# Performance work log

Hardware: AMD Instinct MI355X
Metric: run time of the kernel (lower is better)

The kernel has to match this reference:

```python
import jax, jax.numpy as jnp
import numpy as np

# Layer widths of the hardcoded torch MLP: 2->128->256->512->512->512->512->256->128->3
_DIMS = [2, 128, 256, 512, 512, 512, 512, 256, 128, 3]


def setup_inputs() -> dict:
    key = jax.random.key(0)
    keys = jax.random.split(key, 2 * (len(_DIMS) - 1) + 1)
    inp = {"x": jax.random.uniform(keys[0], (1048576, 2), dtype=jnp.float32)}
    for i in range(len(_DIMS) - 1):
        fan_in, fan_out = _DIMS[i], _DIMS[i + 1]
        bound = 1.0 / np.sqrt(fan_in)  # torch nn.Linear default init range
        inp[f"W{i+1}"] = jax.random.uniform(keys[2 * i + 1], (fan_in, fan_out), jnp.float32, -bound, bound)
        inp[f"b{i+1}"] = jax.random.uniform(keys[2 * i + 2], (fan_out,), jnp.float32, -bound, bound)
    return inp


def reference(x, W1, b1, W2, b2, W3, b3, W4, b4, W5, b5, W6, b6, W7, b7, W8, b8, W9, b9):
    # (transpose of torch's [out, in]); math is identical: y = x @ W + b.
    h = x
    for W, b in ((W1, b1), (W2, b2), (W3, b3), (W4, b4),
                 (W5, b5), (W6, b6), (W7, b7), (W8, b8)):
        h = jax.nn.relu(h @ W + b)
    return jax.nn.sigmoid(h @ W9 + b9)
```

## Files before the change

kernel.cpp:

```cpp
#include <hip/hip_runtime.h>

typedef _Float16 f16;
typedef __attribute__((ext_vector_type(4))) _Float16 f16x4;
typedef __attribute__((ext_vector_type(8))) _Float16 f16x8;
typedef __attribute__((ext_vector_type(16))) float f32x16;

#define MT 128
#define NBF 4
#define LDSP 1024

#define OFF2 0
#define OFF3 32768
#define OFF4 163840
#define OFF5 425984
#define OFF6 688128
#define OFF7 950272
#define OFF8 1081344
#define OFF9 1114112
#define TOTAL_FRAG_LANES 139776

__device__ __forceinline__ uint32_t swz(int row, int colbytes) {
  return (uint32_t)(row * LDSP + (colbytes ^ ((row & 31) << 4)));
}

__global__ void repack_kernel(const float* __restrict__ W2, const float* __restrict__ W3,
                              const float* __restrict__ W4, const float* __restrict__ W5,
                              const float* __restrict__ W6, const float* __restrict__ W7,
                              const float* __restrict__ W8, const float* __restrict__ W9,
                              f16* __restrict__ ws) {
  int gid = blockIdx.x * 256 + threadIdx.x;
  if (gid >= TOTAL_FRAG_LANES) return;
  const float* src; int N, NT; size_t dst; int local;
  if      (gid <   4096) { src = W2; N = 256; NT = 8;  dst = OFF2; local = gid;          }
  else if (gid <  20480) { src = W3; N = 512; NT = 16; dst = OFF3; local = gid -   4096; }
  else if (gid <  53248) { src = W4; N = 512; NT = 16; dst = OFF4; local = gid -  20480; }
  else if (gid <  86016) { src = W5; N = 512; NT = 16; dst = OFF5; local = gid -  53248; }
  else if (gid < 118784) { src = W6; N = 512; NT = 16; dst = OFF6; local = gid -  86016; }
  else if (gid < 135168) { src = W7; N = 256; NT = 8;  dst = OFF7; local = gid - 118784; }
  else if (gid < 139264) { src = W8; N = 128; NT = 4;  dst = OFF8; local = gid - 135168; }
  else                   { src = W9; N = 3;   NT = 1;  dst = OFF9; local = gid - 139264; }
  int lane = local & 63;
  int frag = local >> 6;
  int kf = frag / NT, nf = frag % NT;
  int n  = nf * 32 + (lane & 31);
  int kb = kf * 16 + ((lane >> 5) << 3);
  f16x8 v;
  #pragma unroll
  for (int i = 0; i < 8; ++i) {
    float val = (n < N) ? src[(size_t)(kb + i) * N + n] : 0.0f;
    v[i] = (f16)val;
  }
  *reinterpret_cast<f16x8*>(ws + dst + (size_t)local * 8) = v;
}

template<int KT, int MF, int WMG, int WBG>
__device__ __forceinline__ void run_layer(char* act, const f16* __restrict__ wp,
                                          const float* __restrict__ bias) {
  constexpr int FM  = MF / WMG;
  constexpr int FB  = NBF / WBG;
  const int tid   = threadIdx.x;
  const int lane  = tid & 63;
  const int wid   = tid >> 6;
  const int wm    = wid / WBG;
  const int wb    = wid % WBG;
  const int mlane = lane & 31;
  const int h     = lane >> 5;

  f32x16 acc[FM][FB];
  #pragma unroll
  for (int fm = 0; fm < FM; ++fm) {
    const int mbase = (wm * FM + fm) * 32;
    #pragma unroll
    for (int g = 0; g < 4; ++g) {
      const float4 bb = *reinterpret_cast<const float4*>(&bias[mbase + g * 8 + 4 * h]);
      #pragma unroll
      for (int j = 0; j < 4; ++j)
        #pragma unroll
        for (int fb = 0; fb < FB; ++fb)
          acc[fm][fb][g * 4 + j] = ((const float*)&bb)[j];
    }
  }

  const f16x8* __restrict__ wfrag = reinterpret_cast<const f16x8*>(wp);

  #pragma unroll 2
  for (int kf = 0; kf < KT; ++kf) {
    f16x8 a[FM];
    #pragma unroll
    for (int fm = 0; fm < FM; ++fm)
      a[fm] = wfrag[(size_t)(kf * MF + wm * FM + fm) * 64 + lane];
    f16x8 b[FB];
    #pragma unroll
    for (int fb = 0; fb < FB; ++fb)
      b[fb] = *reinterpret_cast<const f16x8*>(
                  act + swz((wb * FB + fb) * 32 + mlane, kf * 32 + h * 16));
    __builtin_amdgcn_s_setprio(1);
    #pragma unroll
    for (int fm = 0; fm < FM; ++fm)
      #pragma unroll
      for (int fb = 0; fb < FB; ++fb)
        acc[fm][fb] = __builtin_amdgcn_mfma_f32_32x32x16_f16(a[fm], b[fb], acc[fm][fb], 0, 0, 0);
    __builtin_amdgcn_s_setprio(0);
  }

  __syncthreads();
  #pragma unroll
  for (int fm = 0; fm < FM; ++fm) {
    const int mbase = (wm * FM + fm) * 32;
    #pragma unroll
    for (int fb = 0; fb < FB; ++fb) {
      const int row = (wb * FB + fb) * 32 + mlane;
      #pragma unroll
      for (int g = 0; g < 4; ++g) {
        const int m0 = mbase + g * 8 + 4 * h;
        f16x4 v;
        #pragma unroll
        for (int j = 0; j < 4; ++j)
          v[j] = (f16)fmaxf(acc[fm][fb][g * 4 + j], 0.0f);
        *reinterpret_cast<f16x4*>(act + swz(row, m0 * 2)) = v;
      }
    }
  }
  __syncthreads();
}

__global__ __launch_bounds__(512, 2)
void mlp_kernel(const float* __restrict__ x,
                const float* __restrict__ W1, const float* __restrict__ b1,
                const f16*   __restrict__ wpk,
                const float* __restrict__ b2, const float* __restrict__ b3,
                const float* __restrict__ b4, const float* __restrict__ b5,
                const float* __restrict__ b6, const float* __restrict__ b7,
                const float* __restrict__ b8, const float* __restrict__ b9,
                float* __restrict__ out) {
  __shared__ __align__(16) char act[MT * LDSP];
  const int row0 = blockIdx.x * MT;
  const int tid  = threadIdx.x;

  {
    const int r  = tid >> 2;
    const int cb = (tid & 3) * 32;
    const float2 xv = reinterpret_cast<const float2*>(x)[row0 + r];
    #pragma unroll
    for (int q = 0; q < 4; ++q) {
      f16x8 v;
      #pragma unroll
      for (int j = 0; j < 8; ++j) {
        int c = cb + q * 8 + j;
        v[j] = (f16)fmaxf(fmaf(xv.y, W1[128 + c], fmaf(xv.x, W1[c], b1[c])), 0.0f);
      }
      *reinterpret_cast<f16x8*>(act + swz(r, cb * 2 + q * 16)) = v;
    }
  }
  __syncthreads();

  run_layer<8,  8,  4, 2>(act, wpk + OFF2, b2);
  run_layer<16, 16, 4, 2>(act, wpk + OFF3, b3);
  for (int rep = 0; rep < 3; ++rep) {
    const float* bias = (rep == 0) ? b4 : (rep == 1) ? b5 : b6;
    run_layer<32, 16, 4, 2>(act, wpk + OFF4 + rep * (OFF5 - OFF4), bias);
  }
  run_layer<32, 8,  4, 2>(act, wpk + OFF7, b7);
  run_layer<16, 4,  4, 2>(act, wpk + OFF8, b8);

  const int lane = tid & 63;
  const int wid  = tid >> 6;
  if (wid < 4) {
    const int mlane = lane & 31;
    const int h     = lane >> 5;
    f32x16 acc = (f32x16)0.0f;
    const f16x8* __restrict__ wfrag = reinterpret_cast<const f16x8*>(wpk + OFF9);
    #pragma unroll
    for (int kf = 0; kf < 8; ++kf) {
      f16x8 a = wfrag[(size_t)kf * 64 + lane];
      f16x8 b = *reinterpret_cast<const f16x8*>(
                    act + swz(wid * 32 + mlane, kf * 32 + h * 16));
      acc = __builtin_amdgcn_mfma_f32_32x32x16_f16(a, b, acc, 0, 0, 0);
    }
    if (h == 0) {
      const size_t orow = (size_t)(row0 + wid * 32 + mlane) * 3;
      #pragma unroll
      for (int r = 0; r < 3; ++r) {
        float v = acc[r] + b9[r];
        out[orow + r] = 1.0f / (1.0f + __expf(-v));
      }
    }
  }
}

extern "C" void kernel_launch(void* const* d_in, const int* in_sizes, int n_in,
                              void* d_out, int out_size, void* d_ws, size_t ws_size,
                              hipStream_t stream) {
  const float* x  = (const float*)d_in[0];
  const float* W1 = (const float*)d_in[1];  const float* b1 = (const float*)d_in[2];
  const float* W2 = (const float*)d_in[3];  const float* b2 = (const float*)d_in[4];
  const float* W3 = (const float*)d_in[5];  const float* b3 = (const float*)d_in[6];
  const float* W4 = (const float*)d_in[7];  const float* b4 = (const float*)d_in[8];
  const float* W5 = (const float*)d_in[9];  const float* b5 = (const float*)d_in[10];
  const float* W6 = (const float*)d_in[11]; const float* b6 = (const float*)d_in[12];
  const float* W7 = (const float*)d_in[13]; const float* b7 = (const float*)d_in[14];
  const float* W8 = (const float*)d_in[15]; const float* b8 = (const float*)d_in[16];
  const float* W9 = (const float*)d_in[17]; const float* b9 = (const float*)d_in[18];
  f16* wpk = (f16*)d_ws;

  repack_kernel<<<(TOTAL_FRAG_LANES + 255) / 256, 256, 0, stream>>>(
      W2, W3, W4, W5, W6, W7, W8, W9, wpk);

  mlp_kernel<<<1048576 / MT, 512, 0, stream>>>(
      x, W1, b1, wpk, b2, b3, b4, b5, b6, b7, b8, b9, (float*)d_out);
}
```

Baseline: 2.262 ms.

## Stage packed weights into double-buffered LDS via async global_load_lds across layers

```diff
diff --git a/kernel.cpp b/kernel.cpp
--- a/kernel.cpp
+++ b/kernel.cpp
@@ -8,6 +8,7 @@
 #define MT 128
 #define NBF 4
 #define LDSP 1024
+#define WCHUNK 16384
 
 #define OFF2 0
 #define OFF3 32768
@@ -53,12 +54,28 @@
   *reinterpret_cast<f16x8*>(ws + dst + (size_t)local * 8) = v;
 }
 
-template<int KT, int MF, int WMG, int WBG>
-__device__ __forceinline__ void run_layer(char* act, const f16* __restrict__ wp,
-                                          const float* __restrict__ bias) {
-  constexpr int FM  = MF / WMG;
-  constexpr int FB  = NBF / WBG;
-  const int tid   = threadIdx.x;
+__device__ __forceinline__ void gload16(const f16* g, char* l) {
+  __builtin_amdgcn_global_load_lds(
+      (const __attribute__((address_space(1))) void*)g,
+      (__attribute__((address_space(3))) void*)l, 16, 0, 0);
+}
+
+template<int NI>
+__device__ __forceinline__ void stage_chunk(const f16* __restrict__ src, char* dst, int tid) {
+  const int lane = tid & 63, wid = tid >> 6;
+  #pragma unroll
+  for (int i = 0; i < NI; ++i)
+    gload16(src + i * 4096 + wid * 512 + lane * 8, dst + i * 8192 + wid * 1024);
+}
+
+template<int KT, int MF, int WMG, int WBG, int CKF, int NI_NEXT>
+__device__ __forceinline__ void run_layer(char* act, char* wlds,
+                                          const f16* __restrict__ wp,
+                                          const f16* __restrict__ wp_next,
+                                          const float* __restrict__ bias, int tid) {
+  constexpr int NC = KT / CKF;
+  constexpr int FM = MF / WMG;
+  constexpr int FB = NBF / WBG;
   const int lane  = tid & 63;
   const int wid   = tid >> 6;
   const int wm    = wid / WBG;
@@ -81,29 +98,38 @@
     }
   }
 
-  const f16x8* __restrict__ wfrag = reinterpret_cast<const f16x8*>(wp);
-
-  #pragma unroll 2
-  for (int kf = 0; kf < KT; ++kf) {
-    f16x8 a[FM];
-    #pragma unroll
-    for (int fm = 0; fm < FM; ++fm)
-      a[fm] = wfrag[(size_t)(kf * MF + wm * FM + fm) * 64 + lane];
-    f16x8 b[FB];
-    #pragma unroll
-    for (int fb = 0; fb < FB; ++fb)
-      b[fb] = *reinterpret_cast<const f16x8*>(
-                  act + swz((wb * FB + fb) * 32 + mlane, kf * 32 + h * 16));
-    __builtin_amdgcn_s_setprio(1);
-    #pragma unroll
-    for (int fm = 0; fm < FM; ++fm)
+  #pragma unroll 1
+  for (int c = 0; c < NC; ++c) {
+    const int cur = c & 1;
+    if (c + 1 < NC)       stage_chunk<2>(wp + (size_t)(c + 1) * (WCHUNK / 2), wlds + (cur ^ 1) * WCHUNK, tid);
+    else if (NI_NEXT == 2) stage_chunk<2>(wp_next, wlds + (cur ^ 1) * WCHUNK, tid);
+    else if (NI_NEXT == 1) stage_chunk<1>(wp_next, wlds + (cur ^ 1) * WCHUNK, tid);
+    char* wbuf = wlds + cur * WCHUNK;
+    #pragma unroll
+    for (int kk = 0; kk < CKF; ++kk) {
+      const int kf = c * CKF + kk;
+      f16x8 a[FM];
+      #pragma unroll
+      for (int fm = 0; fm < FM; ++fm)
+        a[fm] = *reinterpret_cast<const f16x8*>(wbuf + (kk * MF + wm * FM + fm) * 1024 + lane * 16);
+      f16x8 b[FB];
       #pragma unroll
       for (int fb = 0; fb < FB; ++fb)
-        acc[fm][fb] = __builtin_amdgcn_mfma_f32_32x32x16_f16(a[fm], b[fb], acc[fm][fb], 0, 0, 0);
-    __builtin_amdgcn_s_setprio(0);
-  }
-
-  __syncthreads();
+        b[fb] = *reinterpret_cast<const f16x8*>(
+                    act + swz((wb * FB + fb) * 32 + mlane, kf * 32 + h * 16));
+      __builtin_amdgcn_s_setprio(1);
+      #pragma unroll
+      for (int fm = 0; fm < FM; ++fm)
+        #pragma unroll
+        for (int fb = 0; fb < FB; ++fb)
+          acc[fm][fb] = __builtin_amdgcn_mfma_f32_32x32x16_f16(a[fm], b[fb], acc[fm][fb], 0, 0, 0);
+      __builtin_amdgcn_s_setprio(0);
+    }
+    asm volatile("s_waitcnt vmcnt(0)" ::: "memory");
+    __builtin_amdgcn_s_barrier();
+    asm volatile("" ::: "memory");
+  }
+
   #pragma unroll
   for (int fm = 0; fm < FM; ++fm) {
     const int mbase = (wm * FM + fm) * 32;
@@ -134,8 +160,11 @@
                 const float* __restrict__ b8, const float* __restrict__ b9,
                 float* __restrict__ out) {
   __shared__ __align__(16) char act[MT * LDSP];
+  __shared__ __align__(16) char wlds[2 * WCHUNK];
   const int row0 = blockIdx.x * MT;
   const int tid  = threadIdx.x;
+
+  stage_chunk<2>(wpk + OFF2, wlds, tid);
 
   {
     const int r  = tid >> 2;
@@ -154,14 +183,15 @@
   }
   __syncthreads();
 
-  run_layer<8,  8,  4, 2>(act, wpk + OFF2, b2);
-  run_layer<16, 16, 4, 2>(act, wpk + OFF3, b3);
+  run_layer<8,  8,  8, 1, 2, 2>(act, wlds, wpk + OFF2, wpk + OFF3, b2, tid);
+  run_layer<16, 16, 8, 1, 1, 2>(act, wlds, wpk + OFF3, wpk + OFF4, b3, tid);
   for (int rep = 0; rep < 3; ++rep) {
     const float* bias = (rep == 0) ? b4 : (rep == 1) ? b5 : b6;
-    run_layer<32, 16, 4, 2>(act, wpk + OFF4 + rep * (OFF5 - OFF4), bias);
-  }
-  run_layer<32, 8,  4, 2>(act, wpk + OFF7, b7);
-  run_layer<16, 4,  4, 2>(act, wpk + OFF8, b8);
+    const f16* wp = wpk + OFF4 + rep * (OFF5 - OFF4);
+    run_layer<32, 16, 8, 1, 1, 2>(act, wlds, wp, wp + (OFF5 - OFF4), bias, tid);
+  }
+  run_layer<32, 8,  8, 1, 2, 2>(act, wlds, wpk + OFF7, wpk + OFF8, b7, tid);
+  run_layer<16, 4,  4, 2, 4, 1>(act, wlds, wpk + OFF8, wpk + OFF9, b8, tid);
 
   const int lane = tid & 63;
   const int wid  = tid >> 6;
@@ -169,10 +199,9 @@
     const int mlane = lane & 31;
     const int h     = lane >> 5;
     f32x16 acc = (f32x16)0.0f;
-    const f16x8* __restrict__ wfrag = reinterpret_cast<const f16x8*>(wpk + OFF9);
     #pragma unroll
     for (int kf = 0; kf < 8; ++kf) {
-      f16x8 a = wfrag[(size_t)kf * 64 + lane];
+      f16x8 a = *reinterpret_cast<const f16x8*>(wlds + kf * 1024 + lane * 16);
       f16x8 b = *reinterpret_cast<const f16x8*>(
                     act + swz(wid * 32 + mlane, kf * 32 + h * 16));
       acc = __builtin_amdgcn_mfma_f32_32x32x16_f16(a, b, acc, 0, 0, 0);
```

After: 2.691 ms. 19.0% more time.

## Split tile into two half-tiles and overlap epilogue of one with MFMA loop of other

Applied to the files above, without the earlier changes.

```diff
diff --git a/kernel.cpp b/kernel.cpp
--- a/kernel.cpp
+++ b/kernel.cpp
@@ -5,8 +5,6 @@
 typedef __attribute__((ext_vector_type(8))) _Float16 f16x8;
 typedef __attribute__((ext_vector_type(16))) float f32x16;
 
-#define MT 128
-#define NBF 4
 #define LDSP 1024
 
 #define OFF2 0
@@ -54,19 +52,15 @@
 }
 
 template<int KT, int MF, int WMG, int WBG>
-__device__ __forceinline__ void run_layer(char* act, const f16* __restrict__ wp,
-                                          const float* __restrict__ bias) {
-  constexpr int FM  = MF / WMG;
-  constexpr int FB  = NBF / WBG;
-  const int tid   = threadIdx.x;
-  const int lane  = tid & 63;
-  const int wid   = tid >> 6;
-  const int wm    = wid / WBG;
-  const int wb    = wid % WBG;
-  const int mlane = lane & 31;
-  const int h     = lane >> 5;
-
-  f32x16 acc[FM][FB];
+__device__ __forceinline__ void kloop(const char* actR, const f16* __restrict__ wp,
+                                      const float* __restrict__ bias,
+                                      f32x16 (&acc)[2][2], int tid) {
+  constexpr int FM = MF / WMG;
+  constexpr int FB = 2 / WBG;
+  const int lane = tid & 63, wid = tid >> 6;
+  const int wm = wid / WBG, wb = wid % WBG;
+  const int mlane = lane & 31, h = lane >> 5;
+
   #pragma unroll
   for (int fm = 0; fm < FM; ++fm) {
     const int mbase = (wm * FM + fm) * 32;
@@ -82,7 +76,6 @@
   }
 
   const f16x8* __restrict__ wfrag = reinterpret_cast<const f16x8*>(wp);
-
   #pragma unroll 2
   for (int kf = 0; kf < KT; ++kf) {
     f16x8 a[FM];
@@ -93,7 +86,7 @@
     #pragma unroll
     for (int fb = 0; fb < FB; ++fb)
       b[fb] = *reinterpret_cast<const f16x8*>(
-                  act + swz((wb * FB + fb) * 32 + mlane, kf * 32 + h * 16));
+                  actR + swz((wb * FB + fb) * 32 + mlane, kf * 32 + h * 16));
     __builtin_amdgcn_s_setprio(1);
     #pragma unroll
     for (int fm = 0; fm < FM; ++fm)
@@ -102,8 +95,15 @@
         acc[fm][fb] = __builtin_amdgcn_mfma_f32_32x32x16_f16(a[fm], b[fb], acc[fm][fb], 0, 0, 0);
     __builtin_amdgcn_s_setprio(0);
   }
-
-  __syncthreads();
+}
+
+template<int MF, int WMG, int WBG>
+__device__ __forceinline__ void epi(char* actW, f32x16 (&acc)[2][2], int tid) {
+  constexpr int FM = MF / WMG;
+  constexpr int FB = 2 / WBG;
+  const int lane = tid & 63, wid = tid >> 6;
+  const int wm = wid / WBG, wb = wid % WBG;
+  const int mlane = lane & 31, h = lane >> 5;
   #pragma unroll
   for (int fm = 0; fm < FM; ++fm) {
     const int mbase = (wm * FM + fm) * 32;
@@ -117,11 +117,10 @@
         #pragma unroll
         for (int j = 0; j < 4; ++j)
           v[j] = (f16)fmaxf(acc[fm][fb][g * 4 + j], 0.0f);
-        *reinterpret_cast<f16x4*>(act + swz(row, m0 * 2)) = v;
+        *reinterpret_cast<f16x4*>(actW + swz(row, m0 * 2)) = v;
       }
     }
   }
-  __syncthreads();
 }
 
 __global__ __launch_bounds__(512, 2)
@@ -133,13 +132,18 @@
                 const float* __restrict__ b6, const float* __restrict__ b7,
                 const float* __restrict__ b8, const float* __restrict__ b9,
                 float* __restrict__ out) {
-  __shared__ __align__(16) char act[MT * LDSP];
-  const int row0 = blockIdx.x * MT;
+  __shared__ __align__(16) char actA[64 * LDSP];
+  __shared__ __align__(16) char actB[64 * LDSP];
+  const int row0 = blockIdx.x * 128;
   const int tid  = threadIdx.x;
+
+  f32x16 aA[2][2], aB[2][2];
 
   {
     const int r  = tid >> 2;
     const int cb = (tid & 3) * 32;
+    char* dst = (r < 64) ? actA : actB;
+    const int rr = r & 63;
     const float2 xv = reinterpret_cast<const float2*>(x)[row0 + r];
     #pragma unroll
     for (int q = 0; q < 4; ++q) {
@@ -149,23 +153,53 @@
         int c = cb + q * 8 + j;
         v[j] = (f16)fmaxf(fmaf(xv.y, W1[128 + c], fmaf(xv.x, W1[c], b1[c])), 0.0f);
       }
-      *reinterpret_cast<f16x8*>(act + swz(r, cb * 2 + q * 16)) = v;
-    }
-  }
-  __syncthreads();
-
-  run_layer<8,  8,  4, 2>(act, wpk + OFF2, b2);
-  run_layer<16, 16, 4, 2>(act, wpk + OFF3, b3);
+      *reinterpret_cast<f16x8*>(dst + swz(rr, cb * 2 + q * 16)) = v;
+    }
+  }
+  __syncthreads();
+
+  kloop<8, 8, 8, 1>(actA, wpk + OFF2, b2, aA, tid);
+  __syncthreads();
+  kloop<8, 8, 8, 1>(actB, wpk + OFF2, b2, aB, tid);
+  epi<8, 8, 1>(actA, aA, tid);
+  __syncthreads();
+  kloop<16, 16, 8, 1>(actA, wpk + OFF3, b3, aA, tid);
+  epi<8, 8, 1>(actB, aB, tid);
+  __syncthreads();
+  kloop<16, 16, 8, 1>(actB, wpk + OFF3, b3, aB, tid);
+  epi<16, 8, 1>(actA, aA, tid);
+  __syncthreads();
+  #pragma unroll 1
   for (int rep = 0; rep < 3; ++rep) {
-    const float* bias = (rep == 0) ? b4 : (rep == 1) ? b5 : b6;
-    run_layer<32, 16, 4, 2>(act, wpk + OFF4 + rep * (OFF5 - OFF4), bias);
-  }
-  run_layer<32, 8,  4, 2>(act, wpk + OFF7, b7);
-  run_layer<16, 4,  4, 2>(act, wpk + OFF8, b8);
+    const f16* wp = wpk + OFF4 + rep * (OFF5 - OFF4);
+    const float* bs = (rep == 0) ? b4 : (rep == 1) ? b5 : b6;
+    kloop<32, 16, 8, 1>(actA, wp, bs, aA, tid);
+    epi<16, 8, 1>(actB, aB, tid);
+    __syncthreads();
+    kloop<32, 16, 8, 1>(actB, wp, bs, aB, tid);
+    epi<16, 8, 1>(actA, aA, tid);
+    __syncthreads();
+  }
+  kloop<32, 8, 8, 1>(actA, wpk + OFF7, b7, aA, tid);
+  epi<16, 8, 1>(actB, aB, tid);
+  __syncthreads();
+  kloop<32, 8, 8, 1>(actB, wpk + OFF7, b7, aB, tid);
+  epi<8, 8, 1>(actA, aA, tid);
+  __syncthreads();
+  kloop<16, 4, 4, 2>(actA, wpk + OFF8, b8, aA, tid);
+  epi<8, 8, 1>(actB, aB, tid);
+  __syncthreads();
+  kloop<16, 4, 4, 2>(actB, wpk + OFF8, b8, aB, tid);
+  epi<4, 4, 2>(actA, aA, tid);
+  __syncthreads();
+  epi<4, 4, 2>(actB, aB, tid);
+  __syncthreads();
 
   const int lane = tid & 63;
   const int wid  = tid >> 6;
   if (wid < 4) {
+    const char* tact = (wid < 2) ? actA : actB;
+    const int tw = wid & 1;
     const int mlane = lane & 31;
     const int h     = lane >> 5;
     f32x16 acc = (f32x16)0.0f;
@@ -174,11 +208,11 @@
     for (int kf = 0; kf < 8; ++kf) {
       f16x8 a = wfrag[(size_t)kf * 64 + lane];
       f16x8 b = *reinterpret_cast<const f16x8*>(
-                    act + swz(wid * 32 + mlane, kf * 32 + h * 16));
+                    tact + swz(tw * 32 + mlane, kf * 32 + h * 16));
       acc = __builtin_amdgcn_mfma_f32_32x32x16_f16(a, b, acc, 0, 0, 0);
     }
     if (h == 0) {
-      const size_t orow = (size_t)(row0 + wid * 32 + mlane) * 3;
+      const size_t orow = (size_t)(row0 + (wid >> 1) * 64 + tw * 32 + mlane) * 3;
       #pragma unroll
       for (int r = 0; r < 3; ++r) {
         float v = acc[r] + b9[r];
@@ -206,6 +240,6 @@
   repack_kernel<<<(TOTAL_FRAG_LANES + 255) / 256, 256, 0, stream>>>(
       W2, W3, W4, W5, W6, W7, W8, W9, wpk);
 
-  mlp_kernel<<<1048576 / MT, 512, 0, stream>>>(
+  mlp_kernel<<<1048576 / 128, 512, 0, stream>>>(
       x, W1, b1, wpk, b2, b3, b4, b5, b6, b7, b8, b9, (float*)d_out);
 }
```

Result: slower. 2.694 ms (+19.1%).
